# Kernel tuning notes

Hardware: AMD Instinct MI355X
Metric: run time of the kernel (lower is better)

Reference implementation:

```python
import jax, jax.numpy as jnp
import numpy as np

B, N, D, H = 1, 256, 128, 4
E = D // H  # head dim


def setup_inputs() -> dict:
    key = jax.random.key(0)
    ks = jax.random.split(key, 6)
    s = 0.02
    return {
        "pairwise_repr": jax.random.normal(ks[0], (B, N, N, D), dtype=jnp.float32),
        "mask": jnp.ones((B, N), dtype=bool),
        "Wb": jax.random.normal(ks[1], (D, H), dtype=jnp.float32) * s,
        "Wq": jax.random.normal(ks[2], (D, H * E), dtype=jnp.float32) * s,
        "Wk": jax.random.normal(ks[3], (D, H * E), dtype=jnp.float32) * s,
        "Wv": jax.random.normal(ks[4], (D, H * E), dtype=jnp.float32) * s,
        "Wo": jax.random.normal(ks[5], (H * E, D), dtype=jnp.float32) * s,
    }


def reference(pairwise_repr, mask, Wb, Wq, Wk, Wv, Wo):
    # node_type='starting' -> no transpose. Attention runs over rows: for each
    # row i, attend over column index j (keys k), with a shared per-(b,h) bias
    # computed from the pair representation itself (broadcast over i instead of
    # the torch repeat, same math).
    b, n, _, d = pairwise_repr.shape
    h = Wb.shape[1]
    e = Wq.shape[1] // h
    scale = e ** -0.5

    bias = jnp.einsum('bijd,dh->bhij', pairwise_repr, Wb)           # [b,h,n,n]
    q = jnp.einsum('bijd,dhe->bhije', pairwise_repr, Wq.reshape(d, h, e))
    k = jnp.einsum('bijd,dhe->bhije', pairwise_repr, Wk.reshape(d, h, e))
    v = jnp.einsum('bijd,dhe->bhije', pairwise_repr, Wv.reshape(d, h, e))

    # scores[b,h,i,j,k] = <q_ij, k_ik> * scale + bias[b,h,j,k]
    scores = jnp.einsum('bhije,bhike->bhijk', q, k) * scale
    scores = scores + bias[:, :, None, :, :]
    neg = jnp.asarray(jnp.finfo(scores.dtype).min, scores.dtype)
    scores = jnp.where(mask[:, None, None, None, :], scores, neg)

    attn = jax.nn.softmax(scores, axis=-1)
    o = jnp.einsum('bhijk,bhike->bhije', attn, v)                   # [b,h,n,n,e]
    o = jnp.transpose(o, (0, 2, 3, 1, 4)).reshape(b, n, n, h * e)   # merge heads
    return o @ Wo                                                   # [b,n,n,d]
```

## Files before the change

### kernel.cpp

```cpp
#include <hip/hip_runtime.h>
#include <hip/hip_bf16.h>

namespace {

constexpr int N = 256;
constexpr int D = 128;
constexpr int H = 4;
constexpr int E = 32;
constexpr float SCALE  = 0.17677669529663687f;
constexpr float LOG2E  = 1.4426950408889634f;

constexpr size_t NB_BACC = 0;
constexpr size_t NB_WTT  = NB_BACC + (size_t)H * N * N * 4;
constexpr size_t NB_WOT  = NB_WTT + 3 * (size_t)D * D * 2;
constexpr size_t NEW_NEED = NB_WOT + (size_t)D * D * 2;

typedef __attribute__((ext_vector_type(8)))  short        short8;
typedef __attribute__((ext_vector_type(16))) float        f32x16;
typedef __attribute__((ext_vector_type(4)))  unsigned int uint4v;

#define MFMA(a, b, c) __builtin_amdgcn_mfma_f32_32x32x16_bf16((a), (b), (c), 0, 0, 0)

__device__ inline unsigned short f2bfs(float f) {
  union { __hip_bfloat16 b; unsigned short u; } c;
  c.b = __float2bfloat16(f);
  return c.u;
}
__device__ inline unsigned pack2(float a, float b) {
  return (unsigned)f2bfs(a) | ((unsigned)f2bfs(b) << 16);
}
__device__ inline short8 frag4(unsigned a, unsigned b, unsigned c, unsigned d) {
  union { uint4v u; short8 s; } cv;
  cv.u[0] = a; cv.u[1] = b; cv.u[2] = c; cv.u[3] = d;
  return cv.s;
}

}

__global__ void ta_wt4_kernel(const float* __restrict__ Wq,
                              const float* __restrict__ Wk,
                              const float* __restrict__ Wv,
                              const float* __restrict__ Wo,
                              __hip_bfloat16* __restrict__ wtT,
                              __hip_bfloat16* __restrict__ woT) {
  const int y = blockIdx.y;
  const float* src = (y == 0) ? Wq : (y == 1) ? Wk : (y == 2) ? Wv : Wo;
  __hip_bfloat16* dst = (y < 3) ? (wtT + (size_t)y * D * D) : woT;
  const float sc = (y == 1) ? SCALE : 1.0f;
  int base = blockIdx.x * 1024;
#pragma unroll
  for (int r = 0; r < 4; ++r) {
    int idx = base + r * 256 + (int)threadIdx.x;
    dst[idx] = __float2bfloat16(src[(idx & 127) * D + (idx >> 7)] * sc);
  }
}

__global__ __launch_bounds__(256) void ta_bias_acc_kernel(
    const float* __restrict__ P, const float* __restrict__ Wb,
    float* __restrict__ bacc) {
  __shared__ float wb[D * H];
  int t = threadIdx.x;
  wb[t] = Wb[t];
  wb[t + 256] = Wb[t + 256];
  __syncthreads();

  int j = blockIdx.x;
  int k = t;
  const float4* p4 = reinterpret_cast<const float4*>(P + ((size_t)j * N + k) * D);
  float a0 = 0.f, a1 = 0.f, a2 = 0.f, a3 = 0.f;
#pragma unroll
  for (int d4 = 0; d4 < D / 4; ++d4) {
    float4 p = p4[d4];
    const float* w = &wb[d4 * 16];
    a0 += p.x * w[0] + p.y * w[4] + p.z * w[8]  + p.w * w[12];
    a1 += p.x * w[1] + p.y * w[5] + p.z * w[9]  + p.w * w[13];
    a2 += p.x * w[2] + p.y * w[6] + p.z * w[10] + p.w * w[14];
    a3 += p.x * w[3] + p.y * w[7] + p.z * w[11] + p.w * w[15];
  }
  int kt = k >> 5, kr = k & 31, jt = j >> 5, jc = j & 31;
  int l = jc + 32 * ((kr >> 2) & 1);
  int r = (kr & 3) + 4 * (kr >> 3);
  float av[4] = {a0, a1, a2, a3};
#pragma unroll
  for (int h = 0; h < 4; ++h)
    bacc[((((size_t)h * 8 + kt) * 8 + jt) * 64 + l) * 16 + r] = av[h];
}

__global__ __launch_bounds__(512) void ta_fused_kernel(
    const float* __restrict__ P, const float* __restrict__ bacc,
    const __hip_bfloat16* __restrict__ wtT,
    const __hip_bfloat16* __restrict__ woT,
    float* __restrict__ out) {
  __shared__ __align__(16) unsigned char QO[256 * 80];
  __shared__ __align__(16) unsigned char Ks[256 * 80];
  __shared__ __align__(16) unsigned char Vt[32 * 528];

  const int i = blockIdx.x;
  const int t = threadIdx.x;
  const int w = t >> 6, ln = t & 63, ln31 = ln & 31, hi = ln >> 5;

  short8 af[8];
  {
    const float* prow = P + ((size_t)i * N + 32 * w + ln31) * D;
#pragma unroll
    for (int kc = 0; kc < 8; ++kc) {
      int d0 = 16 * kc + 8 * hi;
      float4 x = *reinterpret_cast<const float4*>(prow + d0);
      float4 y = *reinterpret_cast<const float4*>(prow + d0 + 4);
      short8 r;
      r[0] = (short)f2bfs(x.x); r[1] = (short)f2bfs(x.y);
      r[2] = (short)f2bfs(x.z); r[3] = (short)f2bfs(x.w);
      r[4] = (short)f2bfs(y.x); r[5] = (short)f2bfs(y.y);
      r[6] = (short)f2bfs(y.z); r[7] = (short)f2bfs(y.w);
      af[kc] = r;
    }
  }

  f32x16 oacc[4];
#pragma unroll
  for (int dt = 0; dt < 4; ++dt)
#pragma unroll
    for (int r = 0; r < 16; ++r) oacc[dt][r] = 0.f;

  for (int h = 0; h < H; ++h) {
    f32x16 qa, ka, va;
#pragma unroll
    for (int r = 0; r < 16; ++r) { qa[r] = 0.f; ka[r] = 0.f; va[r] = 0.f; }
#pragma unroll
    for (int kc = 0; kc < 8; ++kc) {
      int d0 = 16 * kc + 8 * hi;
      const __hip_bfloat16* wp = wtT + ((size_t)h * E + ln31) * D + d0;
      short8 bq = *reinterpret_cast<const short8*>(wp);
      short8 bk = *reinterpret_cast<const short8*>(wp + (size_t)D * D);
      short8 bv = *reinterpret_cast<const short8*>(wp + 2 * (size_t)D * D);
      qa = MFMA(af[kc], bq, qa);
      ka = MFMA(af[kc], bk, ka);
      va = MFMA(af[kc], bv, va);
    }
#pragma unroll
    for (int r = 0; r < 16; ++r) {
      int row = 32 * w + (r & 3) + 8 * (r >> 2) + 4 * hi;
      *reinterpret_cast<unsigned short*>(QO + row * 80 + 2 * ln31) = f2bfs(qa[r]);
      *reinterpret_cast<unsigned short*>(Ks + row * 80 + 2 * ln31) = f2bfs(ka[r]);
    }
#pragma unroll
    for (int g = 0; g < 4; ++g) {
      uint2 val;
      val.x = pack2(va[4 * g], va[4 * g + 1]);
      val.y = pack2(va[4 * g + 2], va[4 * g + 3]);
      *reinterpret_cast<uint2*>(Vt + ln31 * 528 + 64 * w + 16 * g + 8 * hi) = val;
    }
    __syncthreads();

    short8 qf0 = *reinterpret_cast<const short8*>(QO + (32 * w + ln31) * 80 + 16 * hi);
    short8 qf1 = *reinterpret_cast<const short8*>(QO + (32 * w + ln31) * 80 + 32 + 16 * hi);

    f32x16 o;
#pragma unroll
    for (int r = 0; r < 16; ++r) o[r] = 0.f;
    float ls = 0.f;

    const float* baccH = bacc + (size_t)h * 8 * 8 * 64 * 16;
    f32x16 bc = *reinterpret_cast<const f32x16*>(baccH + (((size_t)0 * 8 + w) * 64 + ln) * 16);
#pragma unroll
    for (int kt = 0; kt < 8; ++kt) {
      f32x16 bn = bc;
      if (kt < 7)
        bn = *reinterpret_cast<const f32x16*>(
            baccH + (((size_t)(kt + 1) * 8 + w) * 64 + ln) * 16);
      short8 kf0 = *reinterpret_cast<const short8*>(Ks + (32 * kt + ln31) * 80 + 16 * hi);
      short8 kf1 = *reinterpret_cast<const short8*>(Ks + (32 * kt + ln31) * 80 + 32 + 16 * hi);
      short8 vt0 = *reinterpret_cast<const short8*>(Vt + ln31 * 528 + 64 * kt + 16 * hi);
      short8 vt1 = *reinterpret_cast<const short8*>(Vt + ln31 * 528 + 64 * kt + 32 + 16 * hi);

      f32x16 s = bc;
      s = MFMA(kf0, qf0, s);
      s = MFMA(kf1, qf1, s);

      float p[16];
      float lacc = 0.f;
#pragma unroll
      for (int r = 0; r < 16; ++r) { p[r] = exp2f(s[r] * LOG2E); lacc += p[r]; }
      ls += lacc;

      unsigned pk[8], rpk[8];
#pragma unroll
      for (int q = 0; q < 8; ++q) pk[q] = pack2(p[2 * q], p[2 * q + 1]);
#pragma unroll
      for (int q = 0; q < 8; ++q) rpk[q] = __shfl_xor(pk[q], 32);
      short8 pa0 = frag4(hi ? rpk[2] : pk[0], hi ? rpk[3] : pk[1],
                         hi ? pk[2]  : rpk[0], hi ? pk[3]  : rpk[1]);
      short8 pa1 = frag4(hi ? rpk[6] : pk[4], hi ? rpk[7] : pk[5],
                         hi ? pk[6]  : rpk[4], hi ? pk[7]  : rpk[5]);
      o = MFMA(pa0, vt0, o);
      o = MFMA(pa1, vt1, o);
      bc = bn;
    }

    float L = ls + __shfl_xor(ls, 32);
    float Linv = 1.0f / L;
#pragma unroll
    for (int r = 0; r < 16; ++r) {
      int jr = (r & 3) + 8 * (r >> 2) + 4 * hi;
      float Li = __shfl(Linv, jr);
      *reinterpret_cast<unsigned short*>(QO + (32 * w + jr) * 80 + 2 * ln31) =
          f2bfs(o[r] * Li);
    }

#pragma unroll
    for (int kc2 = 0; kc2 < 2; ++kc2) {
      short8 ao = *reinterpret_cast<const short8*>(
          QO + (32 * w + ln31) * 80 + 32 * kc2 + 16 * hi);
#pragma unroll
      for (int dt = 0; dt < 4; ++dt) {
        short8 wof = *reinterpret_cast<const short8*>(
            woT + ((size_t)(32 * dt + ln31)) * D + 32 * h + 16 * kc2 + 8 * hi);
        oacc[dt] = MFMA(ao, wof, oacc[dt]);
      }
    }
    __syncthreads();
  }

#pragma unroll
  for (int dt = 0; dt < 4; ++dt) {
#pragma unroll
    for (int r = 0; r < 16; ++r) {
      int jr = (r & 3) + 8 * (r >> 2) + 4 * hi;
      out[((size_t)i * N + 32 * w + jr) * D + 32 * dt + ln31] = oacc[dt][r];
    }
  }
}

extern "C" void kernel_launch(void* const* d_in, const int* in_sizes, int n_in,
                              void* d_out, int out_size, void* d_ws, size_t ws_size,
                              hipStream_t stream) {
  const float* P  = (const float*)d_in[0];
  const float* Wb = (const float*)d_in[2];
  const float* Wq = (const float*)d_in[3];
  const float* Wk = (const float*)d_in[4];
  const float* Wv = (const float*)d_in[5];
  const float* Wo = (const float*)d_in[6];
  float* out = (float*)d_out;
  char* ws = (char*)d_ws;

  if (ws_size < NEW_NEED) return;

  float* bacc = (float*)(ws + NB_BACC);
  __hip_bfloat16* wtT = (__hip_bfloat16*)(ws + NB_WTT);
  __hip_bfloat16* woT = (__hip_bfloat16*)(ws + NB_WOT);

  ta_wt4_kernel<<<dim3(16, 4), 256, 0, stream>>>(Wq, Wk, Wv, Wo, wtT, woT);
  ta_bias_acc_kernel<<<N, 256, 0, stream>>>(P, Wb, bacc);
  ta_fused_kernel<<<N, 512, 0, stream>>>(P, bacc, wtT, woT, out);
}
```

Measured before the change: 83.50 us.

## Double fused attention block to 16 waves with split-K softmax reduction

Raises the fused kernel from 8 to 16 waves per row block. Q/K projection is assigned to waves 0-7 and V projection to waves 8-15. In attention, each pair of waves splits the 8 key tiles in half, and the partial outputs and row sums are combined through LDS before normalization. The output projection is then split across the wave pair by output column tile. This adds parallelism and latency hiding per block, at the cost of extra barriers, LDS round trips for the partial results, and register pressure under a 1024-thread launch bound.

```diff
diff --git a/kernel.cpp b/kernel.cpp
--- a/kernel.cpp
+++ b/kernel.cpp
@@ -14,6 +14,13 @@
 constexpr size_t NB_WTT  = NB_BACC + (size_t)H * N * N * 4;
 constexpr size_t NB_WOT  = NB_WTT + 3 * (size_t)D * D * 2;
 constexpr size_t NEW_NEED = NB_WOT + (size_t)D * D * 2;
+
+constexpr int KS_OFF = 0;
+constexpr int VT_OFF = 20480;
+constexpr int QO_OFF = 37376;
+constexpr int PO_OFF = 0;
+constexpr int PL_OFF = 32768;
+constexpr int LDS_BYTES = 57856;
 
 typedef __attribute__((ext_vector_type(8)))  short        short8;
 typedef __attribute__((ext_vector_type(16))) float        f32x16;
@@ -86,22 +93,23 @@
     bacc[((((size_t)h * 8 + kt) * 8 + jt) * 64 + l) * 16 + r] = av[h];
 }
 
-__global__ __launch_bounds__(512) void ta_fused_kernel(
+__global__ __launch_bounds__(1024) void ta_fused_kernel(
     const float* __restrict__ P, const float* __restrict__ bacc,
     const __hip_bfloat16* __restrict__ wtT,
     const __hip_bfloat16* __restrict__ woT,
     float* __restrict__ out) {
-  __shared__ __align__(16) unsigned char QO[256 * 80];
-  __shared__ __align__(16) unsigned char Ks[256 * 80];
-  __shared__ __align__(16) unsigned char Vt[32 * 528];
+  __shared__ __align__(16) unsigned char lds[LDS_BYTES];
 
   const int i = blockIdx.x;
   const int t = threadIdx.x;
   const int w = t >> 6, ln = t & 63, ln31 = ln & 31, hi = ln >> 5;
+  const int rt = w & 7;
+  const int u = w >> 1, p = w & 1;
+  const int dt0 = 2 * (w & 1);
 
   short8 af[8];
   {
-    const float* prow = P + ((size_t)i * N + 32 * w + ln31) * D;
+    const float* prow = P + ((size_t)i * N + 32 * rt + ln31) * D;
 #pragma unroll
     for (int kc = 0; kc < 8; ++kc) {
       int d0 = 16 * kc + 8 * hi;
@@ -116,44 +124,55 @@
     }
   }
 
-  f32x16 oacc[4];
-#pragma unroll
-  for (int dt = 0; dt < 4; ++dt)
-#pragma unroll
-    for (int r = 0; r < 16; ++r) oacc[dt][r] = 0.f;
+  f32x16 oacc[2];
+#pragma unroll
+  for (int dd = 0; dd < 2; ++dd)
+#pragma unroll
+    for (int r = 0; r < 16; ++r) oacc[dd][r] = 0.f;
 
   for (int h = 0; h < H; ++h) {
-    f32x16 qa, ka, va;
-#pragma unroll
-    for (int r = 0; r < 16; ++r) { qa[r] = 0.f; ka[r] = 0.f; va[r] = 0.f; }
-#pragma unroll
-    for (int kc = 0; kc < 8; ++kc) {
-      int d0 = 16 * kc + 8 * hi;
-      const __hip_bfloat16* wp = wtT + ((size_t)h * E + ln31) * D + d0;
-      short8 bq = *reinterpret_cast<const short8*>(wp);
-      short8 bk = *reinterpret_cast<const short8*>(wp + (size_t)D * D);
-      short8 bv = *reinterpret_cast<const short8*>(wp + 2 * (size_t)D * D);
-      qa = MFMA(af[kc], bq, qa);
-      ka = MFMA(af[kc], bk, ka);
-      va = MFMA(af[kc], bv, va);
-    }
-#pragma unroll
-    for (int r = 0; r < 16; ++r) {
-      int row = 32 * w + (r & 3) + 8 * (r >> 2) + 4 * hi;
-      *reinterpret_cast<unsigned short*>(QO + row * 80 + 2 * ln31) = f2bfs(qa[r]);
-      *reinterpret_cast<unsigned short*>(Ks + row * 80 + 2 * ln31) = f2bfs(ka[r]);
-    }
-#pragma unroll
-    for (int g = 0; g < 4; ++g) {
-      uint2 val;
-      val.x = pack2(va[4 * g], va[4 * g + 1]);
-      val.y = pack2(va[4 * g + 2], va[4 * g + 3]);
-      *reinterpret_cast<uint2*>(Vt + ln31 * 528 + 64 * w + 16 * g + 8 * hi) = val;
-    }
-    __syncthreads();
-
-    short8 qf0 = *reinterpret_cast<const short8*>(QO + (32 * w + ln31) * 80 + 16 * hi);
-    short8 qf1 = *reinterpret_cast<const short8*>(QO + (32 * w + ln31) * 80 + 32 + 16 * hi);
+    if (w < 8) {
+      f32x16 qa, ka;
+#pragma unroll
+      for (int r = 0; r < 16; ++r) { qa[r] = 0.f; ka[r] = 0.f; }
+#pragma unroll
+      for (int kc = 0; kc < 8; ++kc) {
+        int d0 = 16 * kc + 8 * hi;
+        const __hip_bfloat16* wp = wtT + ((size_t)h * E + ln31) * D + d0;
+        short8 bq = *reinterpret_cast<const short8*>(wp);
+        short8 bk = *reinterpret_cast<const short8*>(wp + (size_t)D * D);
+        qa = MFMA(af[kc], bq, qa);
+        ka = MFMA(af[kc], bk, ka);
+      }
+#pragma unroll
+      for (int r = 0; r < 16; ++r) {
+        int row = 32 * rt + (r & 3) + 8 * (r >> 2) + 4 * hi;
+        *reinterpret_cast<unsigned short*>(lds + QO_OFF + row * 80 + 2 * ln31) = f2bfs(qa[r]);
+        *reinterpret_cast<unsigned short*>(lds + KS_OFF + row * 80 + 2 * ln31) = f2bfs(ka[r]);
+      }
+    } else {
+      f32x16 va;
+#pragma unroll
+      for (int r = 0; r < 16; ++r) va[r] = 0.f;
+#pragma unroll
+      for (int kc = 0; kc < 8; ++kc) {
+        int d0 = 16 * kc + 8 * hi;
+        short8 bv = *reinterpret_cast<const short8*>(
+            wtT + 2 * (size_t)D * D + ((size_t)h * E + ln31) * D + d0);
+        va = MFMA(af[kc], bv, va);
+      }
+#pragma unroll
+      for (int g = 0; g < 4; ++g) {
+        uint2 val;
+        val.x = pack2(va[4 * g], va[4 * g + 1]);
+        val.y = pack2(va[4 * g + 2], va[4 * g + 3]);
+        *reinterpret_cast<uint2*>(lds + VT_OFF + ln31 * 528 + 64 * rt + 16 * g + 8 * hi) = val;
+      }
+    }
+    __syncthreads();
+
+    short8 qf0 = *reinterpret_cast<const short8*>(lds + QO_OFF + (32 * u + ln31) * 80 + 16 * hi);
+    short8 qf1 = *reinterpret_cast<const short8*>(lds + QO_OFF + (32 * u + ln31) * 80 + 32 + 16 * hi);
 
     f32x16 o;
 #pragma unroll
@@ -161,31 +180,33 @@
     float ls = 0.f;
 
     const float* baccH = bacc + (size_t)h * 8 * 8 * 64 * 16;
-    f32x16 bc = *reinterpret_cast<const f32x16*>(baccH + (((size_t)0 * 8 + w) * 64 + ln) * 16);
-#pragma unroll
-    for (int kt = 0; kt < 8; ++kt) {
+    f32x16 bc = *reinterpret_cast<const f32x16*>(
+        baccH + (((size_t)(4 * p) * 8 + u) * 64 + ln) * 16);
+#pragma unroll
+    for (int kk = 0; kk < 4; ++kk) {
+      const int kt = 4 * p + kk;
       f32x16 bn = bc;
-      if (kt < 7)
+      if (kk < 3)
         bn = *reinterpret_cast<const f32x16*>(
-            baccH + (((size_t)(kt + 1) * 8 + w) * 64 + ln) * 16);
-      short8 kf0 = *reinterpret_cast<const short8*>(Ks + (32 * kt + ln31) * 80 + 16 * hi);
-      short8 kf1 = *reinterpret_cast<const short8*>(Ks + (32 * kt + ln31) * 80 + 32 + 16 * hi);
-      short8 vt0 = *reinterpret_cast<const short8*>(Vt + ln31 * 528 + 64 * kt + 16 * hi);
-      short8 vt1 = *reinterpret_cast<const short8*>(Vt + ln31 * 528 + 64 * kt + 32 + 16 * hi);
+            baccH + (((size_t)(kt + 1) * 8 + u) * 64 + ln) * 16);
+      short8 kf0 = *reinterpret_cast<const short8*>(lds + KS_OFF + (32 * kt + ln31) * 80 + 16 * hi);
+      short8 kf1 = *reinterpret_cast<const short8*>(lds + KS_OFF + (32 * kt + ln31) * 80 + 32 + 16 * hi);
+      short8 vt0 = *reinterpret_cast<const short8*>(lds + VT_OFF + ln31 * 528 + 64 * kt + 16 * hi);
+      short8 vt1 = *reinterpret_cast<const short8*>(lds + VT_OFF + ln31 * 528 + 64 * kt + 32 + 16 * hi);
 
       f32x16 s = bc;
       s = MFMA(kf0, qf0, s);
       s = MFMA(kf1, qf1, s);
 
-      float p[16];
+      float pr[16];
       float lacc = 0.f;
 #pragma unroll
-      for (int r = 0; r < 16; ++r) { p[r] = exp2f(s[r] * LOG2E); lacc += p[r]; }
+      for (int r = 0; r < 16; ++r) { pr[r] = exp2f(s[r] * LOG2E); lacc += pr[r]; }
       ls += lacc;
 
       unsigned pk[8], rpk[8];
 #pragma unroll
-      for (int q = 0; q < 8; ++q) pk[q] = pack2(p[2 * q], p[2 * q + 1]);
+      for (int q = 0; q < 8; ++q) pk[q] = pack2(pr[2 * q], pr[2 * q + 1]);
 #pragma unroll
       for (int q = 0; q < 8; ++q) rpk[q] = __shfl_xor(pk[q], 32);
       short8 pa0 = frag4(hi ? rpk[2] : pk[0], hi ? rpk[3] : pk[1],
@@ -196,37 +217,60 @@
       o = MFMA(pa1, vt1, o);
       bc = bn;
     }
-
-    float L = ls + __shfl_xor(ls, 32);
-    float Linv = 1.0f / L;
+    float Lw = ls + __shfl_xor(ls, 32);
+
+    __syncthreads();
+
+    if (p) {
+      float4* dst = reinterpret_cast<float4*>(lds + PO_OFF + u * 4096 + ln * 64);
+#pragma unroll
+      for (int q = 0; q < 4; ++q)
+        dst[q] = make_float4(o[4 * q], o[4 * q + 1], o[4 * q + 2], o[4 * q + 3]);
+      if (ln < 32)
+        *reinterpret_cast<float*>(lds + PL_OFF + u * 128 + 4 * ln) = Lw;
+    }
+    __syncthreads();
+
+    if (!p) {
+      const float4* src = reinterpret_cast<const float4*>(lds + PO_OFF + u * 4096 + ln * 64);
+#pragma unroll
+      for (int q = 0; q < 4; ++q) {
+        float4 v = src[q];
+        o[4 * q + 0] += v.x; o[4 * q + 1] += v.y;
+        o[4 * q + 2] += v.z; o[4 * q + 3] += v.w;
+      }
+      float Lhi = *reinterpret_cast<const float*>(lds + PL_OFF + u * 128 + 4 * ln31);
+      float Linv = 1.0f / (Lw + Lhi);
+#pragma unroll
+      for (int r = 0; r < 16; ++r) {
+        int jr = (r & 3) + 8 * (r >> 2) + 4 * hi;
+        float Li = __shfl(Linv, jr);
+        *reinterpret_cast<unsigned short*>(lds + QO_OFF + (32 * u + jr) * 80 + 2 * ln31) =
+            f2bfs(o[r] * Li);
+      }
+    }
+    __syncthreads();
+
+#pragma unroll
+    for (int kc2 = 0; kc2 < 2; ++kc2) {
+      short8 ao = *reinterpret_cast<const short8*>(
+          lds + QO_OFF + (32 * u + ln31) * 80 + 32 * kc2 + 16 * hi);
+#pragma unroll
+      for (int dd = 0; dd < 2; ++dd) {
+        short8 wof = *reinterpret_cast<const short8*>(
+            woT + ((size_t)(32 * (dt0 + dd) + ln31)) * D + 32 * h + 16 * kc2 + 8 * hi);
+        oacc[dd] = MFMA(ao, wof, oacc[dd]);
+      }
+    }
+    __syncthreads();
+  }
+
+#pragma unroll
+  for (int dd = 0; dd < 2; ++dd) {
 #pragma unroll
     for (int r = 0; r < 16; ++r) {
       int jr = (r & 3) + 8 * (r >> 2) + 4 * hi;
-      float Li = __shfl(Linv, jr);
-      *reinterpret_cast<unsigned short*>(QO + (32 * w + jr) * 80 + 2 * ln31) =
-          f2bfs(o[r] * Li);
-    }
-
-#pragma unroll
-    for (int kc2 = 0; kc2 < 2; ++kc2) {
-      short8 ao = *reinterpret_cast<const short8*>(
-          QO + (32 * w + ln31) * 80 + 32 * kc2 + 16 * hi);
-#pragma unroll
-      for (int dt = 0; dt < 4; ++dt) {
-        short8 wof = *reinterpret_cast<const short8*>(
-            woT + ((size_t)(32 * dt + ln31)) * D + 32 * h + 16 * kc2 + 8 * hi);
-        oacc[dt] = MFMA(ao, wof, oacc[dt]);
-      }
-    }
-    __syncthreads();
-  }
-
-#pragma unroll
-  for (int dt = 0; dt < 4; ++dt) {
-#pragma unroll
-    for (int r = 0; r < 16; ++r) {
-      int jr = (r & 3) + 8 * (r >> 2) + 4 * hi;
-      out[((size_t)i * N + 32 * w + jr) * D + 32 * dt + ln31] = oacc[dt][r];
+      out[((size_t)i * N + 32 * u + jr) * D + 32 * (dt0 + dd) + ln31] = oacc[dd][r];
     }
   }
 }
@@ -251,5 +295,5 @@
 
   ta_wt4_kernel<<<dim3(16, 4), 256, 0, stream>>>(Wq, Wk, Wv, Wo, wtT, woT);
   ta_bias_acc_kernel<<<N, 256, 0, stream>>>(P, Wb, bacc);
-  ta_fused_kernel<<<N, 512, 0, stream>>>(P, bacc, wtT, woT, out);
-}
+  ta_fused_kernel<<<N, 1024, 0, stream>>>(P, bacc, wtT, woT, out);
+}
```

New measurement: 145.5 us. 74.2% more time.

## Double-buffer per-head K/V in LDS and fold log2e into Wk and bias

Applied to the files above, without the earlier changes.

K and V tiles now live in two LDS buffers, and Q and O get their own regions. The next head's Q/K/V projection is issued right after the current head's attention and output projection, so each head needs one barrier instead of two. The P row is reloaded from global memory and converted to bf16 for every head instead of being held in registers, which cuts register pressure but adds repeated global/L2 reads. The softmax scale and log2e are folded into Wk and the bias precompute, removing a multiply per score, and the bias register prefetch is dropped.

```diff
diff --git a/kernel.cpp b/kernel.cpp
--- a/kernel.cpp
+++ b/kernel.cpp
@@ -14,6 +14,14 @@
 constexpr size_t NB_WTT  = NB_BACC + (size_t)H * N * N * 4;
 constexpr size_t NB_WOT  = NB_WTT + 3 * (size_t)D * D * 2;
 constexpr size_t NEW_NEED = NB_WOT + (size_t)D * D * 2;
+
+constexpr int KS_OFF = 0;
+constexpr int KS_SZ  = 256 * 80;
+constexpr int VT_OFF = KS_OFF + 2 * KS_SZ;
+constexpr int VT_SZ  = 32 * 528;
+constexpr int Q_OFF  = VT_OFF + 2 * VT_SZ;
+constexpr int O_OFF  = Q_OFF + 20480;
+constexpr int LDS_BYTES = O_OFF + 20480;
 
 typedef __attribute__((ext_vector_type(8)))  short        short8;
 typedef __attribute__((ext_vector_type(16))) float        f32x16;
@@ -46,7 +54,7 @@
   const int y = blockIdx.y;
   const float* src = (y == 0) ? Wq : (y == 1) ? Wk : (y == 2) ? Wv : Wo;
   __hip_bfloat16* dst = (y < 3) ? (wtT + (size_t)y * D * D) : woT;
-  const float sc = (y == 1) ? SCALE : 1.0f;
+  const float sc = (y == 1) ? SCALE * LOG2E : 1.0f;
   int base = blockIdx.x * 1024;
 #pragma unroll
   for (int r = 0; r < 4; ++r) {
@@ -83,77 +91,79 @@
   float av[4] = {a0, a1, a2, a3};
 #pragma unroll
   for (int h = 0; h < 4; ++h)
-    bacc[((((size_t)h * 8 + kt) * 8 + jt) * 64 + l) * 16 + r] = av[h];
-}
-
-__global__ __launch_bounds__(512) void ta_fused_kernel(
+    bacc[((((size_t)h * 8 + kt) * 8 + jt) * 64 + l) * 16 + r] = av[h] * LOG2E;
+}
+
+__device__ __forceinline__ void stage_head(
+    unsigned char* lds, const float* __restrict__ P,
+    const __hip_bfloat16* __restrict__ wtT,
+    int i, int w, int ln31, int hi, int hh, int buf) {
+  f32x16 qa, ka, va;
+#pragma unroll
+  for (int r = 0; r < 16; ++r) { qa[r] = 0.f; ka[r] = 0.f; va[r] = 0.f; }
+  const float* prow = P + ((size_t)i * N + 32 * w + ln31) * D;
+  const __hip_bfloat16* wbase = wtT + ((size_t)hh * E + ln31) * D;
+#pragma unroll
+  for (int kc = 0; kc < 8; ++kc) {
+    int d0 = 16 * kc + 8 * hi;
+    float4 x = *reinterpret_cast<const float4*>(prow + d0);
+    float4 y = *reinterpret_cast<const float4*>(prow + d0 + 4);
+    short8 a;
+    a[0] = (short)f2bfs(x.x); a[1] = (short)f2bfs(x.y);
+    a[2] = (short)f2bfs(x.z); a[3] = (short)f2bfs(x.w);
+    a[4] = (short)f2bfs(y.x); a[5] = (short)f2bfs(y.y);
+    a[6] = (short)f2bfs(y.z); a[7] = (short)f2bfs(y.w);
+    short8 bq = *reinterpret_cast<const short8*>(wbase + d0);
+    short8 bk = *reinterpret_cast<const short8*>(wbase + (size_t)D * D + d0);
+    short8 bv = *reinterpret_cast<const short8*>(wbase + 2 * (size_t)D * D + d0);
+    qa = MFMA(a, bq, qa);
+    ka = MFMA(a, bk, ka);
+    va = MFMA(a, bv, va);
+  }
+  unsigned char* ksb = lds + KS_OFF + buf * KS_SZ;
+  unsigned char* vtb = lds + VT_OFF + buf * VT_SZ;
+#pragma unroll
+  for (int r = 0; r < 16; ++r) {
+    int row = 32 * w + (r & 3) + 8 * (r >> 2) + 4 * hi;
+    *reinterpret_cast<unsigned short*>(ksb + row * 80 + 2 * ln31) = f2bfs(ka[r]);
+    *reinterpret_cast<unsigned short*>(lds + Q_OFF + row * 80 + 2 * ln31) = f2bfs(qa[r]);
+  }
+#pragma unroll
+  for (int g = 0; g < 4; ++g) {
+    uint2 val;
+    val.x = pack2(va[4 * g], va[4 * g + 1]);
+    val.y = pack2(va[4 * g + 2], va[4 * g + 3]);
+    *reinterpret_cast<uint2*>(vtb + 528 * ln31 + 64 * w + 16 * g + 8 * hi) = val;
+  }
+}
+
+__global__ __launch_bounds__(512, 1) void ta_fused_kernel(
     const float* __restrict__ P, const float* __restrict__ bacc,
     const __hip_bfloat16* __restrict__ wtT,
     const __hip_bfloat16* __restrict__ woT,
     float* __restrict__ out) {
-  __shared__ __align__(16) unsigned char QO[256 * 80];
-  __shared__ __align__(16) unsigned char Ks[256 * 80];
-  __shared__ __align__(16) unsigned char Vt[32 * 528];
+  __shared__ __align__(16) unsigned char lds[LDS_BYTES];
 
   const int i = blockIdx.x;
   const int t = threadIdx.x;
   const int w = t >> 6, ln = t & 63, ln31 = ln & 31, hi = ln >> 5;
 
-  short8 af[8];
-  {
-    const float* prow = P + ((size_t)i * N + 32 * w + ln31) * D;
-#pragma unroll
-    for (int kc = 0; kc < 8; ++kc) {
-      int d0 = 16 * kc + 8 * hi;
-      float4 x = *reinterpret_cast<const float4*>(prow + d0);
-      float4 y = *reinterpret_cast<const float4*>(prow + d0 + 4);
-      short8 r;
-      r[0] = (short)f2bfs(x.x); r[1] = (short)f2bfs(x.y);
-      r[2] = (short)f2bfs(x.z); r[3] = (short)f2bfs(x.w);
-      r[4] = (short)f2bfs(y.x); r[5] = (short)f2bfs(y.y);
-      r[6] = (short)f2bfs(y.z); r[7] = (short)f2bfs(y.w);
-      af[kc] = r;
-    }
-  }
-
   f32x16 oacc[4];
 #pragma unroll
   for (int dt = 0; dt < 4; ++dt)
 #pragma unroll
     for (int r = 0; r < 16; ++r) oacc[dt][r] = 0.f;
 
+  stage_head(lds, P, wtT, i, w, ln31, hi, 0, 0);
+  __syncthreads();
+
   for (int h = 0; h < H; ++h) {
-    f32x16 qa, ka, va;
-#pragma unroll
-    for (int r = 0; r < 16; ++r) { qa[r] = 0.f; ka[r] = 0.f; va[r] = 0.f; }
-#pragma unroll
-    for (int kc = 0; kc < 8; ++kc) {
-      int d0 = 16 * kc + 8 * hi;
-      const __hip_bfloat16* wp = wtT + ((size_t)h * E + ln31) * D + d0;
-      short8 bq = *reinterpret_cast<const short8*>(wp);
-      short8 bk = *reinterpret_cast<const short8*>(wp + (size_t)D * D);
-      short8 bv = *reinterpret_cast<const short8*>(wp + 2 * (size_t)D * D);
-      qa = MFMA(af[kc], bq, qa);
-      ka = MFMA(af[kc], bk, ka);
-      va = MFMA(af[kc], bv, va);
-    }
-#pragma unroll
-    for (int r = 0; r < 16; ++r) {
-      int row = 32 * w + (r & 3) + 8 * (r >> 2) + 4 * hi;
-      *reinterpret_cast<unsigned short*>(QO + row * 80 + 2 * ln31) = f2bfs(qa[r]);
-      *reinterpret_cast<unsigned short*>(Ks + row * 80 + 2 * ln31) = f2bfs(ka[r]);
-    }
-#pragma unroll
-    for (int g = 0; g < 4; ++g) {
-      uint2 val;
-      val.x = pack2(va[4 * g], va[4 * g + 1]);
-      val.y = pack2(va[4 * g + 2], va[4 * g + 3]);
-      *reinterpret_cast<uint2*>(Vt + ln31 * 528 + 64 * w + 16 * g + 8 * hi) = val;
-    }
-    __syncthreads();
-
-    short8 qf0 = *reinterpret_cast<const short8*>(QO + (32 * w + ln31) * 80 + 16 * hi);
-    short8 qf1 = *reinterpret_cast<const short8*>(QO + (32 * w + ln31) * 80 + 32 + 16 * hi);
+    const int b = h & 1;
+    const unsigned char* ksb = lds + KS_OFF + b * KS_SZ;
+    const unsigned char* vtb = lds + VT_OFF + b * VT_SZ;
+
+    short8 qf0 = *reinterpret_cast<const short8*>(lds + Q_OFF + (32 * w + ln31) * 80 + 16 * hi);
+    short8 qf1 = *reinterpret_cast<const short8*>(lds + Q_OFF + (32 * w + ln31) * 80 + 32 + 16 * hi);
 
     f32x16 o;
 #pragma unroll
@@ -161,31 +171,26 @@
     float ls = 0.f;
 
     const float* baccH = bacc + (size_t)h * 8 * 8 * 64 * 16;
-    f32x16 bc = *reinterpret_cast<const f32x16*>(baccH + (((size_t)0 * 8 + w) * 64 + ln) * 16);
 #pragma unroll
     for (int kt = 0; kt < 8; ++kt) {
-      f32x16 bn = bc;
-      if (kt < 7)
-        bn = *reinterpret_cast<const f32x16*>(
-            baccH + (((size_t)(kt + 1) * 8 + w) * 64 + ln) * 16);
-      short8 kf0 = *reinterpret_cast<const short8*>(Ks + (32 * kt + ln31) * 80 + 16 * hi);
-      short8 kf1 = *reinterpret_cast<const short8*>(Ks + (32 * kt + ln31) * 80 + 32 + 16 * hi);
-      short8 vt0 = *reinterpret_cast<const short8*>(Vt + ln31 * 528 + 64 * kt + 16 * hi);
-      short8 vt1 = *reinterpret_cast<const short8*>(Vt + ln31 * 528 + 64 * kt + 32 + 16 * hi);
-
-      f32x16 s = bc;
+      f32x16 s = *reinterpret_cast<const f32x16*>(
+          baccH + (((size_t)kt * 8 + w) * 64 + ln) * 16);
+      short8 kf0 = *reinterpret_cast<const short8*>(ksb + (32 * kt + ln31) * 80 + 16 * hi);
+      short8 kf1 = *reinterpret_cast<const short8*>(ksb + (32 * kt + ln31) * 80 + 32 + 16 * hi);
+      short8 vt0 = *reinterpret_cast<const short8*>(vtb + 528 * ln31 + 64 * kt + 16 * hi);
+      short8 vt1 = *reinterpret_cast<const short8*>(vtb + 528 * ln31 + 64 * kt + 32 + 16 * hi);
+
       s = MFMA(kf0, qf0, s);
       s = MFMA(kf1, qf1, s);
 
-      float p[16];
       float lacc = 0.f;
 #pragma unroll
-      for (int r = 0; r < 16; ++r) { p[r] = exp2f(s[r] * LOG2E); lacc += p[r]; }
+      for (int r = 0; r < 16; ++r) { s[r] = exp2f(s[r]); lacc += s[r]; }
       ls += lacc;
 
       unsigned pk[8], rpk[8];
 #pragma unroll
-      for (int q = 0; q < 8; ++q) pk[q] = pack2(p[2 * q], p[2 * q + 1]);
+      for (int q = 0; q < 8; ++q) pk[q] = pack2(s[2 * q], s[2 * q + 1]);
 #pragma unroll
       for (int q = 0; q < 8; ++q) rpk[q] = __shfl_xor(pk[q], 32);
       short8 pa0 = frag4(hi ? rpk[2] : pk[0], hi ? rpk[3] : pk[1],
@@ -194,7 +199,6 @@
                          hi ? pk[6]  : rpk[4], hi ? pk[7]  : rpk[5]);
       o = MFMA(pa0, vt0, o);
       o = MFMA(pa1, vt1, o);
-      bc = bn;
     }
 
     float L = ls + __shfl_xor(ls, 32);
@@ -203,14 +207,14 @@
     for (int r = 0; r < 16; ++r) {
       int jr = (r & 3) + 8 * (r >> 2) + 4 * hi;
       float Li = __shfl(Linv, jr);
-      *reinterpret_cast<unsigned short*>(QO + (32 * w + jr) * 80 + 2 * ln31) =
+      *reinterpret_cast<unsigned short*>(lds + O_OFF + (32 * w + jr) * 80 + 2 * ln31) =
           f2bfs(o[r] * Li);
     }
 
 #pragma unroll
     for (int kc2 = 0; kc2 < 2; ++kc2) {
       short8 ao = *reinterpret_cast<const short8*>(
-          QO + (32 * w + ln31) * 80 + 32 * kc2 + 16 * hi);
+          lds + O_OFF + (32 * w + ln31) * 80 + 32 * kc2 + 16 * hi);
 #pragma unroll
       for (int dt = 0; dt < 4; ++dt) {
         short8 wof = *reinterpret_cast<const short8*>(
@@ -218,6 +222,10 @@
         oacc[dt] = MFMA(ao, wof, oacc[dt]);
       }
     }
+
+    if (h < 3)
+      stage_head(lds, P, wtT, i, w, ln31, hi, h + 1, (h + 1) & 1);
+
     __syncthreads();
   }
 
```

New measurement: 92.14 us. +10.3%, slower.

## Split fused attention into QKV, per-head attention and projection kernels

Applied to the files above, without the earlier changes.

Replaces the single fused kernel, which looped over the 4 heads inside one block per row, with three kernels. The first computes Q/K/V per row and writes them to global bf16 buffers. The second runs attention with one block per (row, head), giving four times as many blocks. The third applies the output projection. LOG2E is also folded into the Wk scale and the bias, which removes a multiply before each exp2. The goal is more parallelism and shorter serial per-block work, at the cost of tens of MB of extra global round-trip traffic and two more launches; the wtT workspace now aliases the Og buffer.

```diff
diff --git a/kernel.cpp b/kernel.cpp
--- a/kernel.cpp
+++ b/kernel.cpp
@@ -10,10 +10,15 @@
 constexpr float SCALE  = 0.17677669529663687f;
 constexpr float LOG2E  = 1.4426950408889634f;
 
+constexpr size_t SZ_QKV = (size_t)N * H * N * E * 2;
 constexpr size_t NB_BACC = 0;
-constexpr size_t NB_WTT  = NB_BACC + (size_t)H * N * N * 4;
-constexpr size_t NB_WOT  = NB_WTT + 3 * (size_t)D * D * 2;
-constexpr size_t NEW_NEED = NB_WOT + (size_t)D * D * 2;
+constexpr size_t NB_WOT  = NB_BACC + (size_t)H * N * N * 4;
+constexpr size_t NB_QG   = NB_WOT + (size_t)D * D * 2;
+constexpr size_t NB_KG   = NB_QG + SZ_QKV;
+constexpr size_t NB_VG   = NB_KG + SZ_QKV;
+constexpr size_t NB_OG   = NB_VG + SZ_QKV;
+constexpr size_t NB_WTT  = NB_OG;
+constexpr size_t NEW_NEED = NB_OG + SZ_QKV;
 
 typedef __attribute__((ext_vector_type(8)))  short        short8;
 typedef __attribute__((ext_vector_type(16))) float        f32x16;
@@ -46,7 +51,7 @@
   const int y = blockIdx.y;
   const float* src = (y == 0) ? Wq : (y == 1) ? Wk : (y == 2) ? Wv : Wo;
   __hip_bfloat16* dst = (y < 3) ? (wtT + (size_t)y * D * D) : woT;
-  const float sc = (y == 1) ? SCALE : 1.0f;
+  const float sc = (y == 1) ? SCALE * LOG2E : 1.0f;
   int base = blockIdx.x * 1024;
 #pragma unroll
   for (int r = 0; r < 4; ++r) {
@@ -83,17 +88,14 @@
   float av[4] = {a0, a1, a2, a3};
 #pragma unroll
   for (int h = 0; h < 4; ++h)
-    bacc[((((size_t)h * 8 + kt) * 8 + jt) * 64 + l) * 16 + r] = av[h];
-}
-
-__global__ __launch_bounds__(512) void ta_fused_kernel(
-    const float* __restrict__ P, const float* __restrict__ bacc,
-    const __hip_bfloat16* __restrict__ wtT,
-    const __hip_bfloat16* __restrict__ woT,
-    float* __restrict__ out) {
-  __shared__ __align__(16) unsigned char QO[256 * 80];
-  __shared__ __align__(16) unsigned char Ks[256 * 80];
-  __shared__ __align__(16) unsigned char Vt[32 * 528];
+    bacc[((((size_t)h * 8 + kt) * 8 + jt) * 64 + l) * 16 + r] = av[h] * LOG2E;
+}
+
+__global__ __launch_bounds__(512, 2) void ta_qkv_kernel(
+    const float* __restrict__ P, const __hip_bfloat16* __restrict__ wtT,
+    __hip_bfloat16* __restrict__ Qg, __hip_bfloat16* __restrict__ Kg,
+    __hip_bfloat16* __restrict__ Vg) {
+  __shared__ __align__(16) unsigned char lds[3 * 20480];
 
   const int i = blockIdx.x;
   const int t = threadIdx.x;
@@ -116,23 +118,19 @@
     }
   }
 
-  f32x16 oacc[4];
-#pragma unroll
-  for (int dt = 0; dt < 4; ++dt)
-#pragma unroll
-    for (int r = 0; r < 16; ++r) oacc[dt][r] = 0.f;
+  const int crow = t >> 1, chalf = t & 1;
 
   for (int h = 0; h < H; ++h) {
     f32x16 qa, ka, va;
 #pragma unroll
     for (int r = 0; r < 16; ++r) { qa[r] = 0.f; ka[r] = 0.f; va[r] = 0.f; }
+    const __hip_bfloat16* wbase = wtT + ((size_t)h * E + ln31) * D;
 #pragma unroll
     for (int kc = 0; kc < 8; ++kc) {
       int d0 = 16 * kc + 8 * hi;
-      const __hip_bfloat16* wp = wtT + ((size_t)h * E + ln31) * D + d0;
-      short8 bq = *reinterpret_cast<const short8*>(wp);
-      short8 bk = *reinterpret_cast<const short8*>(wp + (size_t)D * D);
-      short8 bv = *reinterpret_cast<const short8*>(wp + 2 * (size_t)D * D);
+      short8 bq = *reinterpret_cast<const short8*>(wbase + d0);
+      short8 bk = *reinterpret_cast<const short8*>(wbase + (size_t)D * D + d0);
+      short8 bv = *reinterpret_cast<const short8*>(wbase + 2 * (size_t)D * D + d0);
       qa = MFMA(af[kc], bq, qa);
       ka = MFMA(af[kc], bk, ka);
       va = MFMA(af[kc], bv, va);
@@ -140,85 +138,157 @@
 #pragma unroll
     for (int r = 0; r < 16; ++r) {
       int row = 32 * w + (r & 3) + 8 * (r >> 2) + 4 * hi;
-      *reinterpret_cast<unsigned short*>(QO + row * 80 + 2 * ln31) = f2bfs(qa[r]);
-      *reinterpret_cast<unsigned short*>(Ks + row * 80 + 2 * ln31) = f2bfs(ka[r]);
-    }
-#pragma unroll
-    for (int g = 0; g < 4; ++g) {
-      uint2 val;
-      val.x = pack2(va[4 * g], va[4 * g + 1]);
-      val.y = pack2(va[4 * g + 2], va[4 * g + 3]);
-      *reinterpret_cast<uint2*>(Vt + ln31 * 528 + 64 * w + 16 * g + 8 * hi) = val;
+      *reinterpret_cast<unsigned short*>(lds +         row * 80 + 2 * ln31) = f2bfs(qa[r]);
+      *reinterpret_cast<unsigned short*>(lds + 20480 + row * 80 + 2 * ln31) = f2bfs(ka[r]);
+      *reinterpret_cast<unsigned short*>(lds + 40960 + row * 80 + 2 * ln31) = f2bfs(va[r]);
     }
     __syncthreads();
 
-    short8 qf0 = *reinterpret_cast<const short8*>(QO + (32 * w + ln31) * 80 + 16 * hi);
-    short8 qf1 = *reinterpret_cast<const short8*>(QO + (32 * w + ln31) * 80 + 32 + 16 * hi);
-
-    f32x16 o;
-#pragma unroll
-    for (int r = 0; r < 16; ++r) o[r] = 0.f;
-    float ls = 0.f;
-
-    const float* baccH = bacc + (size_t)h * 8 * 8 * 64 * 16;
-    f32x16 bc = *reinterpret_cast<const f32x16*>(baccH + (((size_t)0 * 8 + w) * 64 + ln) * 16);
-#pragma unroll
-    for (int kt = 0; kt < 8; ++kt) {
-      f32x16 bn = bc;
-      if (kt < 7)
-        bn = *reinterpret_cast<const f32x16*>(
-            baccH + (((size_t)(kt + 1) * 8 + w) * 64 + ln) * 16);
-      short8 kf0 = *reinterpret_cast<const short8*>(Ks + (32 * kt + ln31) * 80 + 16 * hi);
-      short8 kf1 = *reinterpret_cast<const short8*>(Ks + (32 * kt + ln31) * 80 + 32 + 16 * hi);
-      short8 vt0 = *reinterpret_cast<const short8*>(Vt + ln31 * 528 + 64 * kt + 16 * hi);
-      short8 vt1 = *reinterpret_cast<const short8*>(Vt + ln31 * 528 + 64 * kt + 32 + 16 * hi);
-
-      f32x16 s = bc;
-      s = MFMA(kf0, qf0, s);
-      s = MFMA(kf1, qf1, s);
-
-      float p[16];
-      float lacc = 0.f;
-#pragma unroll
-      for (int r = 0; r < 16; ++r) { p[r] = exp2f(s[r] * LOG2E); lacc += p[r]; }
-      ls += lacc;
-
-      unsigned pk[8], rpk[8];
-#pragma unroll
-      for (int q = 0; q < 8; ++q) pk[q] = pack2(p[2 * q], p[2 * q + 1]);
-#pragma unroll
-      for (int q = 0; q < 8; ++q) rpk[q] = __shfl_xor(pk[q], 32);
-      short8 pa0 = frag4(hi ? rpk[2] : pk[0], hi ? rpk[3] : pk[1],
-                         hi ? pk[2]  : rpk[0], hi ? pk[3]  : rpk[1]);
-      short8 pa1 = frag4(hi ? rpk[6] : pk[4], hi ? rpk[7] : pk[5],
-                         hi ? pk[6]  : rpk[4], hi ? pk[7]  : rpk[5]);
-      o = MFMA(pa0, vt0, o);
-      o = MFMA(pa1, vt1, o);
-      bc = bn;
-    }
-
-    float L = ls + __shfl_xor(ls, 32);
-    float Linv = 1.0f / L;
-#pragma unroll
-    for (int r = 0; r < 16; ++r) {
-      int jr = (r & 3) + 8 * (r >> 2) + 4 * hi;
-      float Li = __shfl(Linv, jr);
-      *reinterpret_cast<unsigned short*>(QO + (32 * w + jr) * 80 + 2 * ln31) =
-          f2bfs(o[r] * Li);
-    }
-
-#pragma unroll
-    for (int kc2 = 0; kc2 < 2; ++kc2) {
-      short8 ao = *reinterpret_cast<const short8*>(
-          QO + (32 * w + ln31) * 80 + 32 * kc2 + 16 * hi);
-#pragma unroll
-      for (int dt = 0; dt < 4; ++dt) {
-        short8 wof = *reinterpret_cast<const short8*>(
-            woT + ((size_t)(32 * dt + ln31)) * D + 32 * h + 16 * kc2 + 8 * hi);
-        oacc[dt] = MFMA(ao, wof, oacc[dt]);
+    const size_t gbase = ((size_t)(i * H + h) * N + crow) * E;
+#pragma unroll
+    for (int m = 0; m < 3; ++m) {
+      __hip_bfloat16* dst = (m == 0) ? Qg : (m == 1) ? Kg : Vg;
+#pragma unroll
+      for (int c = 0; c < 2; ++c) {
+        short8 v = *reinterpret_cast<const short8*>(
+            lds + m * 20480 + crow * 80 + 32 * chalf + 16 * c);
+        *reinterpret_cast<short8*>(dst + gbase + 16 * chalf + 8 * c) = v;
       }
     }
     __syncthreads();
+  }
+}
+
+__global__ __launch_bounds__(512, 2) void ta_attn_kernel(
+    const __hip_bfloat16* __restrict__ Qg, const __hip_bfloat16* __restrict__ Kg,
+    const __hip_bfloat16* __restrict__ Vg, const float* __restrict__ bacc,
+    __hip_bfloat16* __restrict__ Og) {
+  constexpr int KS_OFF = 0;
+  constexpr int VT_OFF = 20480;
+  __shared__ __align__(16) unsigned char lds[20480 + 16896];
+
+  const int i = blockIdx.x >> 2;
+  const int h = blockIdx.x & 3;
+  const int t = threadIdx.x;
+  const int w = t >> 6, ln = t & 63, ln31 = ln & 31, hi = ln >> 5;
+  const size_t base = (size_t)(i * H + h) * N * E;
+
+  {
+    const int row = t >> 1, half = t & 1;
+#pragma unroll
+    for (int c = 0; c < 2; ++c) {
+      short8 kv = *reinterpret_cast<const short8*>(Kg + base + row * E + 16 * half + 8 * c);
+      *reinterpret_cast<short8*>(lds + KS_OFF + row * 80 + 32 * half + 16 * c) = kv;
+    }
+    short8 v0 = *reinterpret_cast<const short8*>(Vg + base + row * E + 16 * half);
+    short8 v1 = *reinterpret_cast<const short8*>(Vg + base + row * E + 16 * half + 8);
+#pragma unroll
+    for (int e = 0; e < 8; ++e) {
+      *reinterpret_cast<unsigned short*>(lds + VT_OFF + (16 * half + e) * 528 + 2 * row) =
+          (unsigned short)v0[e];
+      *reinterpret_cast<unsigned short*>(lds + VT_OFF + (16 * half + 8 + e) * 528 + 2 * row) =
+          (unsigned short)v1[e];
+    }
+  }
+  const int qrow = 32 * w + ln31;
+  short8 qf0 = *reinterpret_cast<const short8*>(Qg + base + qrow * E + 8 * hi);
+  short8 qf1 = *reinterpret_cast<const short8*>(Qg + base + qrow * E + 16 + 8 * hi);
+  __syncthreads();
+
+  f32x16 o;
+#pragma unroll
+  for (int r = 0; r < 16; ++r) o[r] = 0.f;
+  float ls = 0.f;
+
+  const float* baccH = bacc + (size_t)h * 8 * 8 * 64 * 16;
+  f32x16 bc = *reinterpret_cast<const f32x16*>(baccH + (((size_t)0 * 8 + w) * 64 + ln) * 16);
+#pragma unroll
+  for (int kt = 0; kt < 8; ++kt) {
+    f32x16 bn = bc;
+    if (kt < 7)
+      bn = *reinterpret_cast<const f32x16*>(
+          baccH + (((size_t)(kt + 1) * 8 + w) * 64 + ln) * 16);
+    short8 kf0 = *reinterpret_cast<const short8*>(lds + KS_OFF + (32 * kt + ln31) * 80 + 16 * hi);
+    short8 kf1 = *reinterpret_cast<const short8*>(lds + KS_OFF + (32 * kt + ln31) * 80 + 32 + 16 * hi);
+    short8 vt0 = *reinterpret_cast<const short8*>(lds + VT_OFF + 528 * ln31 + 64 * kt + 16 * hi);
+    short8 vt1 = *reinterpret_cast<const short8*>(lds + VT_OFF + 528 * ln31 + 64 * kt + 32 + 16 * hi);
+
+    f32x16 s = bc;
+    s = MFMA(kf0, qf0, s);
+    s = MFMA(kf1, qf1, s);
+
+    float lacc = 0.f;
+#pragma unroll
+    for (int r = 0; r < 16; ++r) { s[r] = exp2f(s[r]); lacc += s[r]; }
+    ls += lacc;
+
+    unsigned pk[8], rpk[8];
+#pragma unroll
+    for (int q = 0; q < 8; ++q) pk[q] = pack2(s[2 * q], s[2 * q + 1]);
+#pragma unroll
+    for (int q = 0; q < 8; ++q) rpk[q] = __shfl_xor(pk[q], 32);
+    short8 pa0 = frag4(hi ? rpk[2] : pk[0], hi ? rpk[3] : pk[1],
+                       hi ? pk[2]  : rpk[0], hi ? pk[3]  : rpk[1]);
+    short8 pa1 = frag4(hi ? rpk[6] : pk[4], hi ? rpk[7] : pk[5],
+                       hi ? pk[6]  : rpk[4], hi ? pk[7]  : rpk[5]);
+    o = MFMA(pa0, vt0, o);
+    o = MFMA(pa1, vt1, o);
+    bc = bn;
+  }
+
+  float L = ls + __shfl_xor(ls, 32);
+  float Linv = 1.0f / L;
+
+  __syncthreads();
+
+#pragma unroll
+  for (int r = 0; r < 16; ++r) {
+    int jr = (r & 3) + 8 * (r >> 2) + 4 * hi;
+    float Li = __shfl(Linv, jr);
+    *reinterpret_cast<unsigned short*>(lds + KS_OFF + (32 * w + jr) * 80 + 2 * ln31) =
+        f2bfs(o[r] * Li);
+  }
+  __syncthreads();
+
+  {
+    const int row = t >> 1, half = t & 1;
+#pragma unroll
+    for (int c = 0; c < 2; ++c) {
+      short8 v = *reinterpret_cast<const short8*>(
+          lds + KS_OFF + row * 80 + 32 * half + 16 * c);
+      *reinterpret_cast<short8*>(Og + base + row * E + 16 * half + 8 * c) = v;
+    }
+  }
+}
+
+__global__ __launch_bounds__(512, 2) void ta_proj_kernel(
+    const __hip_bfloat16* __restrict__ Og, const __hip_bfloat16* __restrict__ woT,
+    float* __restrict__ out) {
+  const int i = blockIdx.x;
+  const int t = threadIdx.x;
+  const int w = t >> 6, ln = t & 63, ln31 = ln & 31, hi = ln >> 5;
+  const int row = 32 * w + ln31;
+
+  short8 af[8];
+#pragma unroll
+  for (int kc = 0; kc < 8; ++kc)
+    af[kc] = *reinterpret_cast<const short8*>(
+        Og + ((size_t)(i * H + (kc >> 1)) * N + row) * E + 16 * (kc & 1) + 8 * hi);
+
+  f32x16 oacc[4];
+#pragma unroll
+  for (int dt = 0; dt < 4; ++dt)
+#pragma unroll
+    for (int r = 0; r < 16; ++r) oacc[dt][r] = 0.f;
+
+#pragma unroll
+  for (int kc = 0; kc < 8; ++kc) {
+#pragma unroll
+    for (int dt = 0; dt < 4; ++dt) {
+      short8 wof = *reinterpret_cast<const short8*>(
+          woT + ((size_t)(32 * dt + ln31)) * D + 16 * kc + 8 * hi);
+      oacc[dt] = MFMA(af[kc], wof, oacc[dt]);
+    }
   }
 
 #pragma unroll
@@ -246,10 +316,16 @@
   if (ws_size < NEW_NEED) return;
 
   float* bacc = (float*)(ws + NB_BACC);
+  __hip_bfloat16* woT = (__hip_bfloat16*)(ws + NB_WOT);
   __hip_bfloat16* wtT = (__hip_bfloat16*)(ws + NB_WTT);
-  __hip_bfloat16* woT = (__hip_bfloat16*)(ws + NB_WOT);
+  __hip_bfloat16* Qg  = (__hip_bfloat16*)(ws + NB_QG);
+  __hip_bfloat16* Kg  = (__hip_bfloat16*)(ws + NB_KG);
+  __hip_bfloat16* Vg  = (__hip_bfloat16*)(ws + NB_VG);
+  __hip_bfloat16* Og  = (__hip_bfloat16*)(ws + NB_OG);
 
   ta_wt4_kernel<<<dim3(16, 4), 256, 0, stream>>>(Wq, Wk, Wv, Wo, wtT, woT);
   ta_bias_acc_kernel<<<N, 256, 0, stream>>>(P, Wb, bacc);
-  ta_fused_kernel<<<N, 512, 0, stream>>>(P, bacc, wtT, woT, out);
-}
+  ta_qkv_kernel<<<N, 512, 0, stream>>>(P, wtT, Qg, Kg, Vg);
+  ta_attn_kernel<<<N * H, 512, 0, stream>>>(Qg, Kg, Vg, bacc, Og);
+  ta_proj_kernel<<<N, 512, 0, stream>>>(Og, woT, out);
+}
```

Result: slower. 111.4 us (+33.4%).
